# Optimization experiments

Measured on AMD Instinct MI355X. Metric: run time of the kernel, lower is better.

Reference implementation:

```python
import jax, jax.numpy as jnp
import numpy as np
import math

B, S, HID = 2, 2048, 4096
H, HD = 32, HID // 32  # num_heads, head_dim


def setup_inputs() -> dict:
    key = jax.random.key(0)
    ks = jax.random.split(key, 7)
    hidden_states = jax.random.normal(ks[0], (B, S, HID), jnp.float32)
    residual = jax.random.normal(ks[1], (B, S, HID), jnp.float32)
    # BLOOM alibi: [B*H, 1, kv_len]; realistic slopes * positions
    slopes = jnp.asarray(2.0 ** (-8.0 * (np.arange(1, H + 1) / H)), jnp.float32)  # [H]
    alibi = (slopes[:, None] * jnp.arange(S, dtype=jnp.float32)[None, :])  # [H, S]
    alibi = jnp.broadcast_to(alibi[None], (B, H, S)).reshape(B * H, 1, S)
    # causal mask: True = masked (upper triangle)
    causal = ~jnp.tril(jnp.ones((S, S), bool))
    attention_mask = jnp.broadcast_to(causal[None, None], (B, 1, S, S))
    Wqkv = jax.random.normal(ks[2], (HID, 3 * HID), jnp.float32) * 0.02
    bqkv = jax.random.normal(ks[3], (3 * HID,), jnp.float32) * 0.02
    Wd = jax.random.normal(ks[4], (HID, HID), jnp.float32) * 0.02
    bd = jax.random.normal(ks[5], (HID,), jnp.float32) * 0.02
    return {"hidden_states": hidden_states, "residual": residual, "alibi": alibi,
            "attention_mask": attention_mask, "Wqkv": Wqkv, "bqkv": bqkv,
            "Wd": Wd, "bd": bd}


def reference(hidden_states, residual, alibi, attention_mask, Wqkv, bqkv, Wd, bd):
    b, s, _ = hidden_states.shape
    inv_norm = 1.0 / math.sqrt(HD)
    fused = hidden_states @ Wqkv + bqkv                       # [b,s,3*HID]
    fused = fused.reshape(b, s, H, 3, HD)
    q = jnp.transpose(fused[..., 0, :], (0, 2, 1, 3))         # [b,H,s,hd]
    k = jnp.transpose(fused[..., 1, :], (0, 2, 1, 3))
    v = jnp.transpose(fused[..., 2, :], (0, 2, 1, 3))
    # baddbmm: alibi + inv_norm * q @ k^T
    scores = jnp.einsum('bhqd,bhkd->bhqk', q, k) * inv_norm
    scores = scores + alibi.reshape(b, H, 1, s)               # broadcast over q
    neg = jnp.finfo(jnp.float32).min
    scores = jnp.where(attention_mask, neg, scores)
    probs = jax.nn.softmax(scores.astype(jnp.float32), axis=-1)
    ctx = jnp.einsum('bhqk,bhkd->bhqd', probs, v)             # [b,H,s,hd]
    ctx = jnp.transpose(ctx, (0, 2, 1, 3)).reshape(b, s, HID)
    out = ctx @ Wd + bd
    return residual + out
```

## Files before the change

kernel.cpp:

```cpp
#include <hip/hip_runtime.h>
#include <cstdint>
#include <cstddef>


typedef unsigned short u16;
typedef unsigned int u32;
typedef __bf16 bf16x8 __attribute__((ext_vector_type(8)));
typedef float f32x4 __attribute__((ext_vector_type(4)));
typedef u16 u16x4 __attribute__((ext_vector_type(4)));

#define LDS_AS(p) ((__attribute__((address_space(3))) u32*)(p))
#define GLB_AS(p) ((__attribute__((address_space(1))) u32*)(p))

__device__ __forceinline__ void load16(const void* g, void* l) {
  __builtin_amdgcn_global_load_lds(GLB_AS(g), LDS_AS(l), 16, 0, 0);
}

__device__ __forceinline__ u16 f2bf(float f) {
  union { float f; u32 u; } x; x.f = f;
  u32 r = x.u + 0x7fffu + ((x.u >> 16) & 1u);
  return (u16)(r >> 16);
}

__global__ __launch_bounds__(256) void cvt_bf16(const float* __restrict__ in,
                                                u16* __restrict__ out, int n) {
  int i = (blockIdx.x * 256 + threadIdx.x) * 4;
  if (i >= n) return;
  float4 v = *(const float4*)(in + i);
  u16x4 o = { f2bf(v.x), f2bf(v.y), f2bf(v.z), f2bf(v.w) };
  *(u16x4*)(out + i) = o;
}

__global__ __launch_bounds__(256) void cvt_transpose(const float* __restrict__ W,
                                                     u16* __restrict__ WT,
                                                     int K, int N) {
  __shared__ float tile[32][33];
  int n0 = blockIdx.x * 32, k0 = blockIdx.y * 32;
  int tx = threadIdx.x & 31, ty = threadIdx.x >> 5;
  for (int r = ty; r < 32; r += 8)
    tile[r][tx] = W[(size_t)(k0 + r) * N + n0 + tx];
  __syncthreads();
  for (int r = ty; r < 32; r += 8)
    WT[(size_t)(n0 + r) * K + k0 + tx] = f2bf(tile[tx][r]);
}

__global__ __launch_bounds__(256) void transpose_v(const u16* __restrict__ fused,
                                                   u16* __restrict__ vt) {
  __shared__ __align__(16) u16 tile[64][136];
  int st = blockIdx.x * 64, bh = blockIdx.y;
  int b = bh >> 5, h = bh & 31;
  int tx = threadIdx.x & 15, ty = threadIdx.x >> 4;
  for (int r = ty; r < 64; r += 16) {
    const u16* src = fused + (size_t)(b * 2048 + st + r) * 12288 + h * 384 + 256 + tx * 8;
    u16x4 a = *(const u16x4*)(src);
    u16x4 c = *(const u16x4*)(src + 4);
    *(u16x4*)&tile[r][tx * 8] = a;
    *(u16x4*)&tile[r][tx * 8 + 4] = c;
  }
  __syncthreads();
  for (int d = ty; d < 128; d += 16) {
    u16x4 o = { tile[tx * 4 + 0][d], tile[tx * 4 + 1][d],
                tile[tx * 4 + 2][d], tile[tx * 4 + 3][d] };
    *(u16x4*)(vt + ((size_t)bh * 128 + d) * 2048 + st + tx * 4) = o;
  }
}

template <int EPI>
__global__ __launch_bounds__(256) void gemm_bt(const u16* __restrict__ A,
                                               const u16* __restrict__ BT,
                                               const float* __restrict__ bias,
                                               const float* __restrict__ res,
                                               void* __restrict__ out,
                                               int M, int N, int K) {
  __shared__ __align__(16) u16 As[128 * 32];
  __shared__ __align__(16) u16 Bs[128 * 32];
  const int tid = threadIdx.x, wave = tid >> 6, lane = tid & 63;
  const int quad = lane >> 4, l16 = lane & 15;
  const int m0 = blockIdx.y * 128, n0 = blockIdx.x * 128;
  const int wm = (wave >> 1) * 64, wn = (wave & 1) * 64;

  const f32x4 fz = {0.f, 0.f, 0.f, 0.f};
  f32x4 acc[4][4];
  for (int i = 0; i < 4; ++i)
    for (int j = 0; j < 4; ++j) acc[i][j] = fz;

  const int i0 = wave * 2;
  const int t0 = i0 * 1024 + lane * 16;
  const int t1 = t0 + 1024;
  const int rA0 = t0 >> 6, cA0 = t0 & 63;
  const int rA1 = t1 >> 6, cA1 = t1 & 63;

  for (int k0 = 0; k0 < K; k0 += 32) {
    __syncthreads();
    load16((const char*)(A + (size_t)(m0 + rA0) * K + k0) + cA0, (char*)As + i0 * 1024);
    load16((const char*)(A + (size_t)(m0 + rA1) * K + k0) + cA1, (char*)As + i0 * 1024 + 1024);
    load16((const char*)(BT + (size_t)(n0 + rA0) * K + k0) + cA0, (char*)Bs + i0 * 1024);
    load16((const char*)(BT + (size_t)(n0 + rA1) * K + k0) + cA1, (char*)Bs + i0 * 1024 + 1024);
    __syncthreads();

    bf16x8 af[4], bfv[4];
    for (int i = 0; i < 4; ++i)
      af[i] = *(const bf16x8*)((const char*)As + ((wm + i * 16 + l16) * 32 + quad * 8) * 2);
    for (int j = 0; j < 4; ++j)
      bfv[j] = *(const bf16x8*)((const char*)Bs + ((wn + j * 16 + l16) * 32 + quad * 8) * 2);
    for (int i = 0; i < 4; ++i)
      for (int j = 0; j < 4; ++j)
        acc[i][j] = __builtin_amdgcn_mfma_f32_16x16x32_bf16(af[i], bfv[j], acc[i][j], 0, 0, 0);
  }

  for (int i = 0; i < 4; ++i) {
    int row = m0 + wm + i * 16 + quad * 4;
    for (int j = 0; j < 4; ++j) {
      int col = n0 + wn + j * 16 + l16;
      float bv = bias[col];
      for (int t = 0; t < 4; ++t) {
        float v = acc[i][j][t] + bv;
        size_t idx = (size_t)(row + t) * N + col;
        if (EPI == 1) {
          ((float*)out)[idx] = v + res[idx];
        } else {
          ((u16*)out)[idx] = f2bf(v);
        }
      }
    }
  }
}

__global__ __launch_bounds__(256) void flash_attn(const u16* __restrict__ fused,
                                                  const u16* __restrict__ vt,
                                                  const float* __restrict__ alibi,
                                                  u16* __restrict__ ctx) {
  __shared__ __align__(16) u16 Kbuf[2][64 * 128];
  __shared__ __align__(16) u16 Vbuf[128 * 64];
  __shared__ __align__(16) u16 Ps[64 * 72];

  const int tid = threadIdx.x, wave = tid >> 6, lane = tid & 63;
  const int quad = lane >> 4, l16 = lane & 15;
  const int qt = blockIdx.x, bh = blockIdx.y;
  const int b = bh >> 5, h = bh & 31;
  const int q0 = qt * 64;
  const float scale = 0.08838834764831845f;
  const f32x4 fz = {0.f, 0.f, 0.f, 0.f};

  const u16* srcQ[4];
  const u16* srcK[4];
  for (int j = 0; j < 4; ++j) {
    int inst = wave * 4 + j;
    int row = inst * 4 + quad;
    int cg = l16 ^ (row & 15);
    srcQ[j] = fused + (size_t)(b * 2048 + q0 + row) * 12288 + h * 384 + cg * 8;
    srcK[j] = fused + (size_t)(b * 2048 + row) * 12288 + h * 384 + 128 + cg * 8;
  }
  const u16* srcV[4];
  for (int j = 0; j < 4; ++j) {
    int inst = wave * 4 + j;
    int row = inst * 8 + (lane >> 3);
    int cg = (lane & 7) ^ (row & 7);
    srcV[j] = vt + ((size_t)bh * 128 + row) * 2048 + cg * 8;
  }

  for (int j = 0; j < 4; ++j) {
    int inst = wave * 4 + j;
    load16(srcQ[j], (char*)Kbuf[1] + inst * 1024);
    load16(srcK[j], (char*)Kbuf[0] + inst * 1024);
  }
  __syncthreads();

  bf16x8 qf[4];
  for (int kk = 0; kk < 4; ++kk) {
    int row = wave * 16 + l16;
    int cs = (kk * 4 + quad) ^ l16;
    qf[kk] = *(const bf16x8*)((const char*)Kbuf[1] + row * 256 + cs * 16);
  }
  __syncthreads();

  float m_st[4] = {-__builtin_inff(), -__builtin_inff(), -__builtin_inff(), -__builtin_inff()};
  float l_st[4] = {0.f, 0.f, 0.f, 0.f};
  f32x4 o_acc[8];
  for (int f = 0; f < 8; ++f) o_acc[f] = fz;

  const int nkv = qt + 1;
  for (int kvt = 0; kvt < nkv; ++kvt) {
    const int kv0 = kvt * 64;
    const int cur = kvt & 1;

    for (int j = 0; j < 4; ++j) {
      int inst = wave * 4 + j;
      load16(srcV[j] + kv0, (char*)Vbuf + inst * 1024);
    }
    if (kvt + 1 < nkv) {
      for (int j = 0; j < 4; ++j) {
        int inst = wave * 4 + j;
        load16(srcK[j] + (size_t)(kv0 + 64) * 12288, (char*)Kbuf[cur ^ 1] + inst * 1024);
      }
    }

    f32x4 sa[4];
    for (int j = 0; j < 4; ++j) sa[j] = fz;
    for (int kk = 0; kk < 4; ++kk) {
      for (int j = 0; j < 4; ++j) {
        int row = j * 16 + l16;
        int cs = (kk * 4 + quad) ^ l16;
        bf16x8 bv = *(const bf16x8*)((const char*)Kbuf[cur] + row * 256 + cs * 16);
        sa[j] = __builtin_amdgcn_mfma_f32_16x16x32_bf16(qf[kk], bv, sa[j], 0, 0, 0);
      }
    }

    float al[4];
    for (int j = 0; j < 4; ++j) al[j] = alibi[(size_t)bh * 2048 + kv0 + j * 16 + l16];
    float p[4][4];
    const bool diag = (kvt == qt);
    for (int j = 0; j < 4; ++j) {
      int kvg = kv0 + j * 16 + l16;
      for (int t = 0; t < 4; ++t) {
        float v = sa[j][t] * scale + al[j];
        if (diag) {
          int qg = q0 + wave * 16 + quad * 4 + t;
          if (kvg > qg) v = -__builtin_inff();
        }
        p[j][t] = v;
      }
    }

    float mnew[4], alpha[4];
    for (int t = 0; t < 4; ++t) {
      float mx = fmaxf(fmaxf(p[0][t], p[1][t]), fmaxf(p[2][t], p[3][t]));
      for (int off = 1; off < 16; off <<= 1) mx = fmaxf(mx, __shfl_xor(mx, off, 64));
      mnew[t] = fmaxf(m_st[t], mx);
      alpha[t] = __expf(m_st[t] - mnew[t]);
      m_st[t] = mnew[t];
      float rs = 0.f;
      for (int j = 0; j < 4; ++j) {
        p[j][t] = __expf(p[j][t] - mnew[t]);
        rs += p[j][t];
      }
      for (int off = 1; off < 16; off <<= 1) rs += __shfl_xor(rs, off, 64);
      l_st[t] = l_st[t] * alpha[t] + rs;
    }
    for (int f = 0; f < 8; ++f)
      for (int t = 0; t < 4; ++t) o_acc[f][t] *= alpha[t];

    for (int j = 0; j < 4; ++j)
      for (int t = 0; t < 4; ++t)
        Ps[(wave * 16 + quad * 4 + t) * 72 + j * 16 + l16] = f2bf(p[j][t]);

    __syncthreads();

    for (int kk = 0; kk < 2; ++kk) {
      bf16x8 a = *(const bf16x8*)((const char*)Ps + ((wave * 16 + l16) * 72 + kk * 32 + quad * 8) * 2);
      for (int f = 0; f < 8; ++f) {
        int row = f * 16 + l16;
        int cs = (kk * 4 + quad) ^ (l16 & 7);
        bf16x8 bv = *(const bf16x8*)((const char*)Vbuf + row * 128 + cs * 16);
        o_acc[f] = __builtin_amdgcn_mfma_f32_16x16x32_bf16(a, bv, o_acc[f], 0, 0, 0);
      }
    }

    __syncthreads();
  }

  float invl[4];
  for (int t = 0; t < 4; ++t) invl[t] = 1.0f / l_st[t];
  for (int f = 0; f < 8; ++f) {
    int d = h * 128 + f * 16 + l16;
    for (int t = 0; t < 4; ++t) {
      int row = b * 2048 + q0 + wave * 16 + quad * 4 + t;
      ctx[(size_t)row * 4096 + d] = f2bf(o_acc[f][t] * invl[t]);
    }
  }
}

extern "C" void kernel_launch(void* const* d_in, const int* in_sizes, int n_in,
                              void* d_out, int out_size, void* d_ws, size_t ws_size,
                              hipStream_t stream) {
  const float* hs    = (const float*)d_in[0];
  const float* resid = (const float*)d_in[1];
  const float* alibi = (const float*)d_in[2];
  const float* Wqkv  = (const float*)d_in[4];
  const float* bqkv  = (const float*)d_in[5];
  const float* Wd    = (const float*)d_in[6];
  const float* bd    = (const float*)d_in[7];

  char* ws = (char*)d_ws;
  u16* Abf   = (u16*)(ws);
  u16* W1T   = (u16*)(ws + (size_t)33554432);
  u16* fused = (u16*)(ws + (size_t)134217728);
  u16* vtb   = (u16*)(ws + (size_t)234881024);
  u16* ctx   = (u16*)(ws);
  u16* W2T   = (u16*)(ws + (size_t)33554432);

  cvt_bf16<<<16384, 256, 0, stream>>>(hs, Abf, 16777216);
  cvt_transpose<<<dim3(384, 128), 256, 0, stream>>>(Wqkv, W1T, 4096, 12288);
  gemm_bt<0><<<dim3(96, 32), 256, 0, stream>>>(Abf, W1T, bqkv, nullptr, fused, 4096, 12288, 4096);
  transpose_v<<<dim3(32, 64), 256, 0, stream>>>(fused, vtb);
  cvt_transpose<<<dim3(128, 128), 256, 0, stream>>>(Wd, W2T, 4096, 4096);
  flash_attn<<<dim3(32, 64), 256, 0, stream>>>(fused, vtb, alibi, ctx);
  gemm_bt<1><<<dim3(32, 32), 256, 0, stream>>>(ctx, W2T, bd, resid, d_out, 4096, 4096, 4096);
}
```

Before: 1.510 ms.

## Replace 128x128 GEMM with 256x256 double-buffered, swizzled, 8-wave pipelined GEMM

```diff
diff --git a/kernel.cpp b/kernel.cpp
--- a/kernel.cpp
+++ b/kernel.cpp
@@ -66,56 +66,127 @@
 }
 
 template <int EPI>
-__global__ __launch_bounds__(256) void gemm_bt(const u16* __restrict__ A,
-                                               const u16* __restrict__ BT,
-                                               const float* __restrict__ bias,
-                                               const float* __restrict__ res,
-                                               void* __restrict__ out,
-                                               int M, int N, int K) {
-  __shared__ __align__(16) u16 As[128 * 32];
-  __shared__ __align__(16) u16 Bs[128 * 32];
+__global__ __launch_bounds__(512, 2) void gemm256(const u16* __restrict__ A,
+                                                  const u16* __restrict__ BT,
+                                                  const float* __restrict__ bias,
+                                                  const float* __restrict__ res,
+                                                  void* __restrict__ out,
+                                                  int M, int N, int K) {
+  __shared__ __align__(16) u16 lds[2][4][8192];
+  char* ldsB = (char*)lds;
+
   const int tid = threadIdx.x, wave = tid >> 6, lane = tid & 63;
   const int quad = lane >> 4, l16 = lane & 15;
-  const int m0 = blockIdx.y * 128, n0 = blockIdx.x * 128;
-  const int wm = (wave >> 1) * 64, wn = (wave & 1) * 64;
+  const int wr = wave >> 2, wc = wave & 3;
+
+  const int nwg = gridDim.x, per = nwg >> 3, bid = blockIdx.x;
+  const int swz = (bid & 7) * per + (bid >> 3);
+  const int ntn = N >> 8;
+  const int tm = swz / ntn, tn = swz - tm * ntn;
+  const int m0 = tm << 8, n0 = tn << 8;
+
+  const int r0 = wave * 8 + (lane >> 3);
+  const int scb = ((lane & 7) ^ ((lane >> 3) & 7)) << 4;
+  const char* Ab = (const char*)A;
+  const char* Bb = (const char*)BT;
+  const size_t ROW64 = (size_t)K * 128;
+  size_t aOff[2], bOff[2];
+#pragma unroll
+  for (int h = 0; h < 2; ++h) {
+    aOff[h] = ((size_t)(m0 + h * 128 + r0) * K) * 2 + scb;
+    bOff[h] = ((size_t)(n0 + h * 128 + r0) * K) * 2 + scb;
+  }
+
+#define STAGE_A(b, h, kt) do {                                                  \
+    char* d_ = ldsB + (((b) * 4 + (h)) * 16384) + wave * 1024;                  \
+    load16(Ab + aOff[h] + (size_t)(kt) * 128, d_);                              \
+    load16(Ab + aOff[h] + ROW64 + (size_t)(kt) * 128, d_ + 8192);               \
+  } while (0)
+#define STAGE_B(b, h, kt) do {                                                  \
+    char* d_ = ldsB + (((b) * 4 + 2 + (h)) * 16384) + wave * 1024;              \
+    load16(Bb + bOff[h] + (size_t)(kt) * 128, d_);                              \
+    load16(Bb + bOff[h] + ROW64 + (size_t)(kt) * 128, d_ + 8192);               \
+  } while (0)
+
+  const int sw = (l16 & 7) << 4;
+  const int ca0 = (quad * 16) ^ sw;
+  const int ca1 = (64 + quad * 16) ^ sw;
+  const char* aBase = ldsB + wr * 16384 + l16 * 128;
+  const char* bBase = ldsB + (2 + (wc >> 1)) * 16384 + ((wc & 1) * 64 + l16) * 128;
 
   const f32x4 fz = {0.f, 0.f, 0.f, 0.f};
-  f32x4 acc[4][4];
-  for (int i = 0; i < 4; ++i)
+  f32x4 acc[8][4];
+#pragma unroll
+  for (int i = 0; i < 8; ++i)
+#pragma unroll
     for (int j = 0; j < 4; ++j) acc[i][j] = fz;
-
-  const int i0 = wave * 2;
-  const int t0 = i0 * 1024 + lane * 16;
-  const int t1 = t0 + 1024;
-  const int rA0 = t0 >> 6, cA0 = t0 & 63;
-  const int rA1 = t1 >> 6, cA1 = t1 & 63;
-
-  for (int k0 = 0; k0 < K; k0 += 32) {
-    __syncthreads();
-    load16((const char*)(A + (size_t)(m0 + rA0) * K + k0) + cA0, (char*)As + i0 * 1024);
-    load16((const char*)(A + (size_t)(m0 + rA1) * K + k0) + cA1, (char*)As + i0 * 1024 + 1024);
-    load16((const char*)(BT + (size_t)(n0 + rA0) * K + k0) + cA0, (char*)Bs + i0 * 1024);
-    load16((const char*)(BT + (size_t)(n0 + rA1) * K + k0) + cA1, (char*)Bs + i0 * 1024 + 1024);
-    __syncthreads();
-
-    bf16x8 af[4], bfv[4];
-    for (int i = 0; i < 4; ++i)
-      af[i] = *(const bf16x8*)((const char*)As + ((wm + i * 16 + l16) * 32 + quad * 8) * 2);
-    for (int j = 0; j < 4; ++j)
-      bfv[j] = *(const bf16x8*)((const char*)Bs + ((wn + j * 16 + l16) * 32 + quad * 8) * 2);
-    for (int i = 0; i < 4; ++i)
-      for (int j = 0; j < 4; ++j)
-        acc[i][j] = __builtin_amdgcn_mfma_f32_16x16x32_bf16(af[i], bfv[j], acc[i][j], 0, 0, 0);
-  }
-
-  for (int i = 0; i < 4; ++i) {
-    int row = m0 + wm + i * 16 + quad * 4;
-    for (int j = 0; j < 4; ++j) {
-      int col = n0 + wn + j * 16 + l16;
-      float bv = bias[col];
+  bf16x8 af[8], bfv[8];
+
+#define LDA(b, mb) do {                                                         \
+    _Pragma("unroll") for (int m4 = 0; m4 < 4; ++m4) {                          \
+      af[m4 * 2 + 0] = *(const bf16x8*)(aBase + (b) * 65536 + ((mb) + m4) * 2048 + ca0); \
+      af[m4 * 2 + 1] = *(const bf16x8*)(aBase + (b) * 65536 + ((mb) + m4) * 2048 + ca1); \
+    } } while (0)
+#define LDB_ALL(b) do {                                                         \
+    _Pragma("unroll") for (int n4 = 0; n4 < 4; ++n4) {                          \
+      bfv[n4 * 2 + 0] = *(const bf16x8*)(bBase + (b) * 65536 + n4 * 2048 + ca0); \
+      bfv[n4 * 2 + 1] = *(const bf16x8*)(bBase + (b) * 65536 + n4 * 2048 + ca1); \
+    } } while (0)
+#define MMQ(mh, nh) do {                                                        \
+    __builtin_amdgcn_s_setprio(1);                                              \
+    _Pragma("unroll") for (int m4 = 0; m4 < 4; ++m4)                            \
+    _Pragma("unroll") for (int n2 = 0; n2 < 2; ++n2)                            \
+    _Pragma("unroll") for (int kk = 0; kk < 2; ++kk)                            \
+      acc[(mh) * 4 + m4][(nh) * 2 + n2] = __builtin_amdgcn_mfma_f32_16x16x32_bf16( \
+          af[m4 * 2 + kk], bfv[((nh) * 2 + n2) * 2 + kk],                       \
+          acc[(mh) * 4 + m4][(nh) * 2 + n2], 0, 0, 0);                          \
+    __builtin_amdgcn_s_setprio(0);                                              \
+  } while (0)
+#define BAR() __builtin_amdgcn_s_barrier()
+#define VMCNT6() asm volatile("s_waitcnt vmcnt(6)" ::: "memory")
+
+  STAGE_B(0, 0, 0); STAGE_B(0, 1, 0);
+  STAGE_A(0, 0, 0); STAGE_A(0, 1, 0);
+  STAGE_B(1, 0, 1); STAGE_B(1, 1, 1);
+  STAGE_A(1, 0, 1);
+  VMCNT6();
+  BAR();
+
+  const int NIT = K >> 7;
+#pragma unroll 1
+  for (int i = 0; i < NIT; ++i) {
+    const int t0 = i * 2;
+    LDA(0, 0); LDB_ALL(0); STAGE_A(1, 1, t0 + 1); BAR(); MMQ(0, 0); BAR();
+    STAGE_B(0, 0, t0 + 2); BAR(); MMQ(0, 1); BAR();
+    LDA(0, 4); STAGE_B(0, 1, t0 + 2); BAR(); MMQ(1, 0); BAR();
+    STAGE_A(0, 0, t0 + 2); VMCNT6(); BAR(); MMQ(1, 1); BAR();
+    LDA(1, 0); LDB_ALL(1); STAGE_A(0, 1, t0 + 2); BAR(); MMQ(0, 0); BAR();
+    STAGE_B(1, 0, t0 + 3); BAR(); MMQ(0, 1); BAR();
+    LDA(1, 4); STAGE_B(1, 1, t0 + 3); BAR(); MMQ(1, 0); BAR();
+    STAGE_A(1, 0, t0 + 3); VMCNT6(); BAR(); MMQ(1, 1); BAR();
+  }
+
+#undef STAGE_A
+#undef STAGE_B
+#undef LDA
+#undef LDB_ALL
+#undef MMQ
+#undef BAR
+#undef VMCNT6
+
+  const int row0 = m0 + wr * 128 + quad * 4;
+  const int col0 = n0 + wc * 64 + l16;
+#pragma unroll
+  for (int m = 0; m < 8; ++m) {
+    const int rb = row0 + m * 16;
+#pragma unroll
+    for (int n = 0; n < 4; ++n) {
+      const int col = col0 + n * 16;
+      const float bv = bias[col];
+#pragma unroll
       for (int t = 0; t < 4; ++t) {
-        float v = acc[i][j][t] + bv;
-        size_t idx = (size_t)(row + t) * N + col;
+        float v = acc[m][n][t] + bv;
+        size_t idx = (size_t)(rb + t) * N + col;
         if (EPI == 1) {
           ((float*)out)[idx] = v + res[idx];
         } else {
@@ -291,9 +362,9 @@
 
   cvt_bf16<<<16384, 256, 0, stream>>>(hs, Abf, 16777216);
   cvt_transpose<<<dim3(384, 128), 256, 0, stream>>>(Wqkv, W1T, 4096, 12288);
-  gemm_bt<0><<<dim3(96, 32), 256, 0, stream>>>(Abf, W1T, bqkv, nullptr, fused, 4096, 12288, 4096);
+  gemm256<0><<<dim3(768), 512, 0, stream>>>(Abf, W1T, bqkv, nullptr, fused, 4096, 12288, 4096);
   transpose_v<<<dim3(32, 64), 256, 0, stream>>>(fused, vtb);
   cvt_transpose<<<dim3(128, 128), 256, 0, stream>>>(Wd, W2T, 4096, 4096);
   flash_attn<<<dim3(32, 64), 256, 0, stream>>>(fused, vtb, alibi, ctx);
-  gemm_bt<1><<<dim3(32, 32), 256, 0, stream>>>(ctx, W2T, bd, resid, d_out, 4096, 4096, 4096);
-}
+  gemm256<1><<<dim3(256), 512, 0, stream>>>(ctx, W2T, bd, resid, d_out, 4096, 4096, 4096);
+}
```

Result: no change. 1.521 ms (+0.7%).
